# Performance work log

Measured on AMD Instinct MI355X. Metric: run time of the kernel, lower is better.

The kernel has to match this reference:

```python
import jax, jax.numpy as jnp
import numpy as np


def _cft_icft_matrices(n):
    # Continuous FT over t in [0,1) sampled at n points, frequencies = fftfreq(n, d=1/n).
    # CFT  : X(f) = integral x(t) e^{-2pi i f t} dt  ~=  (1/n) * sum_t x(t) e^{-2pi i f t}
    # ICFT : x(t) = integral X(f) e^{+2pi i f t} df  ~=  df   * sum_f X(f) e^{+2pi i f t}
    # The original module evaluates the ICFT on the fftshift-ed frequency grid while the
    # coefficients stay in fft (unshifted) index order; we reproduce that pairing.
    sr = float(n)
    t = jnp.arange(n, dtype=jnp.float32) / n                      # [n]
    f = jnp.fft.fftfreq(n, d=1.0 / sr).astype(jnp.float32)        # [n], fft order
    f_shift = jnp.fft.fftshift(f)                                 # [n], shifted order
    two_pi = jnp.float32(2.0 * np.pi)
    dt = jnp.float32(1.0 / n)
    df = jnp.float32(sr / n)  # frequency spacing = 1.0 for unit duration
    # E_cft: [n_freq, n_time], E_icft: [n_time, n_freq]
    E_cft = jnp.exp(-1j * two_pi * f[:, None] * t[None, :]).astype(jnp.complex64) * dt
    E_icft = jnp.exp(1j * two_pi * t[:, None] * f_shift[None, :]).astype(jnp.complex64) * df
    return E_cft, E_icft


def setup_inputs() -> dict:
    key = jax.random.key(0)
    k1, k2, k3 = jax.random.split(key, 3)
    B, Ci, Co, n, modes = 32, 64, 64, 4096, 64
    scale = 1.0 / (Ci * Co)
    x = jax.random.normal(k1, (B, Ci, n), dtype=jnp.float32)
    # weights1 = scale * rand(Ci, Co, modes, cfloat): uniform[0,1) real and imag parts
    w_real = scale * jax.random.uniform(k2, (Ci, Co, modes), dtype=jnp.float32)
    w_imag = scale * jax.random.uniform(k3, (Ci, Co, modes), dtype=jnp.float32)
    return {"x": x, "w_real": w_real, "w_imag": w_imag}


def reference(x, w_real, w_imag):
    B, Ci, n = x.shape
    Co, modes = w_real.shape[1], w_real.shape[2]
    E_cft, E_icft = _cft_icft_matrices(n)
    w = (w_real + 1j * w_imag).astype(jnp.complex64)              # [Ci, Co, modes]
    xc = x.astype(jnp.complex64)
    # Batched CFT over all (batch, channel) pairs as one complex GEMM.
    x_cft = jnp.einsum('bit,ft->bif', xc, E_cft)                  # [B, Ci, n]
    # Spectral linear transform on the lowest `modes` frequencies.
    low = jnp.einsum('bif,iof->bof', x_cft[:, :, :modes], w)      # [B, Co, modes]
    out_ft = jnp.zeros((B, Co, n), dtype=jnp.complex64).at[:, :, :modes].set(low)
    # Batched ICFT back to the time grid; module returns the real part.
    out = jnp.einsum('bof,tf->bot', out_ft, E_icft)               # [B, Co, n]
    return out.real
```

## Files before the change

### kernel.cpp

```cpp
#include <hip/hip_runtime.h>
#include <math.h>

#define NT 4096
#define MODES 64
#define ROWS 2048
#define TWO_PI 6.283185307179586f

typedef __attribute__((ext_vector_type(8))) short bf16x8;
typedef __attribute__((ext_vector_type(4))) float f32x4;

static __device__ __forceinline__ unsigned short bf16rn(float x) {
  unsigned u = __float_as_uint(x);
  u += 0x7FFFu + ((u >> 16) & 1u);
  return (unsigned short)(u >> 16);
}

__global__ __launch_bounds__(256) void bgen_kernel(unsigned short* __restrict__ Bg,
                                                   unsigned short* __restrict__ Cg) {
  const int bx = (int)blockIdx.x;
  if (bx < 256) {
    const int e0 = (bx * 256 + (int)threadIdx.x) * 8;
    const int n = e0 >> 12;
    const int t0 = e0 & 4095;
    const int k = (n < 64) ? n : (n - 64);
    bf16x8 pack;
#pragma unroll
    for (int j = 0; j < 8; ++j) {
      const int ph = (k * (t0 + j)) & (NT - 1);
      float s, c;
      sincosf(TWO_PI * (float)ph / (float)NT, &s, &c);
      const float v = ((n < 64) ? c : -s) * (1.0f / (float)NT);
      pack[j] = (short)bf16rn(v);
    }
    *(bf16x8*)(Bg + e0) = pack;
  } else {
    const int e0 = ((bx - 256) * 256 + (int)threadIdx.x) * 8;
    const int t = e0 >> 7;
    const int k2b = e0 & 127;
    const float sgn = (t & 1) ? -1.f : 1.f;
    bf16x8 pack;
#pragma unroll
    for (int j = 0; j < 8; ++j) {
      const int k2 = k2b + j;
      const int k = (k2 < 64) ? k2 : (k2 - 64);
      const int ph = (k * t) & (NT - 1);
      float s, c;
      sincosf(TWO_PI * (float)ph / (float)NT, &s, &c);
      const float v = ((k2 < 64) ? c : -s) * sgn;
      pack[j] = (short)bf16rn(v);
    }
    *(bf16x8*)(Cg + e0) = pack;
  }
}

__global__ __launch_bounds__(256) void cft_mfma_kernel(
    const float* __restrict__ x, const unsigned short* __restrict__ Bg,
    float* __restrict__ xfp,
    const float* __restrict__ w_real, const float* __restrict__ w_imag,
    float* __restrict__ wrt, float* __restrict__ wit, int S) {
  __shared__ __align__(16) char smem[24576];
  const int tid = threadIdx.x;
  const int nCft = 64 * S;

  if ((int)blockIdx.x >= nCft) {
    float (*tile)[65] = (float (*)[65])smem;
    const int bx = (int)blockIdx.x - nCft;
    const int sel = bx >> 6;
    const int io0 = (bx & 63) * 64;
    const float* __restrict__ src = sel ? w_imag : w_real;
    float* __restrict__ dst = sel ? wit : wrt;
#pragma unroll
    for (int j = 0; j < 4; ++j) {
      const int idx = tid + j * 256;
      const int r = idx >> 4;
      const int kq = idx & 15;
      float4 v = ((const float4*)src)[(size_t)(io0 + r) * 16 + kq];
      tile[r][4 * kq + 0] = v.x; tile[r][4 * kq + 1] = v.y;
      tile[r][4 * kq + 2] = v.z; tile[r][4 * kq + 3] = v.w;
    }
    __syncthreads();
#pragma unroll
    for (int j = 0; j < 16; ++j) {
      const int idx = tid + j * 256;
      const int k = idx >> 6;
      const int r = idx & 63;
      dst[(size_t)k * 4096 + io0 + r] = tile[r][k];
    }
    return;
  }

  unsigned short* Ah = (unsigned short*)smem;
  unsigned short* Al = (unsigned short*)(smem + 4096);
  unsigned short* Bs = (unsigned short*)(smem + 8192);

  const int rowblk = (int)blockIdx.x / S;
  const int ts = (int)blockIdx.x % S;
  const int row0 = rowblk * 32;
  const int t0 = ts * (NT / S);
  const int subs = (NT / S) / 64;

  const int lane = tid & 63;
  const int w = tid >> 6;

  f32x4 acc[2][2];
#pragma unroll
  for (int mt = 0; mt < 2; ++mt)
#pragma unroll
    for (int nt = 0; nt < 2; ++nt) acc[mt][nt] = (f32x4){0.f, 0.f, 0.f, 0.f};

  const int aru = tid & 7;
  const int arow = tid >> 3;

  for (int sub = 0; sub < subs; ++sub) {
    const int tb = t0 + sub * 64;
    __syncthreads();
    {
      const float* xp = x + (size_t)(row0 + arow) * NT + tb + aru * 8;
      const float4 v0 = *(const float4*)xp;
      const float4 v1 = *(const float4*)(xp + 4);
      float xv[8] = {v0.x, v0.y, v0.z, v0.w, v1.x, v1.y, v1.z, v1.w};
      bf16x8 ph, pl;
#pragma unroll
      for (int j = 0; j < 8; ++j) {
        const unsigned short h = bf16rn(xv[j]);
        ph[j] = (short)h;
        const float hf = __uint_as_float((unsigned)h << 16);
        pl[j] = (short)bf16rn(xv[j] - hf);
      }
      const int col = (aru ^ (arow & 7)) * 8;
      *(bf16x8*)(Ah + arow * 64 + col) = ph;
      *(bf16x8*)(Al + arow * 64 + col) = pl;
    }
#pragma unroll
    for (int it = 0; it < 4; ++it) {
      const int idx = tid + it * 256;
      const int ku = idx & 7;
      const int n = idx >> 3;
      const bf16x8 v = *(const bf16x8*)(Bg + (size_t)n * NT + tb + ku * 8);
      const int col = (ku ^ (n & 7)) * 8;
      *(bf16x8*)(Bs + n * 64 + col) = v;
    }
    __syncthreads();
    const int kg = lane >> 4;
#pragma unroll
    for (int ks = 0; ks < 2; ++ks) {
      bf16x8 bf[2];
#pragma unroll
      for (int nt = 0; nt < 2; ++nt) {
        const int n = w * 32 + nt * 16 + (lane & 15);
        const int col = ((ks * 4 + kg) ^ (n & 7)) * 8;
        bf[nt] = *(const bf16x8*)(Bs + n * 64 + col);
      }
#pragma unroll
      for (int mt = 0; mt < 2; ++mt) {
        const int row = mt * 16 + (lane & 15);
        const int col = ((ks * 4 + kg) ^ (row & 7)) * 8;
        const bf16x8 ah = *(const bf16x8*)(Ah + row * 64 + col);
        const bf16x8 al = *(const bf16x8*)(Al + row * 64 + col);
#pragma unroll
        for (int nt = 0; nt < 2; ++nt) {
          acc[mt][nt] = __builtin_amdgcn_mfma_f32_16x16x32_bf16(ah, bf[nt], acc[mt][nt], 0, 0, 0);
          acc[mt][nt] = __builtin_amdgcn_mfma_f32_16x16x32_bf16(al, bf[nt], acc[mt][nt], 0, 0, 0);
        }
      }
    }
  }
  const int nb = w * 32 + (lane & 15);
#pragma unroll
  for (int nt = 0; nt < 2; ++nt) {
    const int n = nb + nt * 16;
    const int plane = n >> 6;
    const int kk = n & 63;
#pragma unroll
    for (int mt = 0; mt < 2; ++mt) {
      const int rl = mt * 16 + (lane >> 4) * 4;
      float4 st = {acc[mt][nt][0], acc[mt][nt][1], acc[mt][nt][2], acc[mt][nt][3]};
      ((float4*)xfp)[((((size_t)ts * 64 + rowblk) * 2 + plane) * 64 + kk) * 8 + (rl >> 2)] = st;
    }
  }
}

__global__ __launch_bounds__(256) void mix_kernel(
    const float* __restrict__ wrt, const float* __restrict__ wit,
    const float* __restrict__ xfp, float2* __restrict__ yf_t, int S) {
  __shared__ float2 wsc[4096];
  __shared__ float2 xsh[256];
  const int k = blockIdx.x & 63;
  const int bq = blockIdx.x >> 6;
  const int tid = threadIdx.x;
#pragma unroll
  for (int j = 0; j < 4; ++j) {
    const int idx = tid + 256 * j;
    float4 vr = ((const float4*)(wrt + (size_t)k * 4096))[idx];
    float4 vi = ((const float4*)(wit + (size_t)k * 4096))[idx];
    wsc[4 * idx + 0] = make_float2(vr.x, vi.x);
    wsc[4 * idx + 1] = make_float2(vr.y, vi.y);
    wsc[4 * idx + 2] = make_float2(vr.z, vi.z);
    wsc[4 * idx + 3] = make_float2(vr.w, vi.w);
  }
  {
    const int R = bq * 256 + tid;
    const int rowblk = R >> 5;
    const int rl = R & 31;
    float2 acc = make_float2(0.f, 0.f);
    for (int s = 0; s < S; ++s) {
      const size_t b0 = (((size_t)s * 64 + rowblk) * 2) * 2048;
      acc.x += xfp[b0 + (size_t)k * 32 + rl];
      acc.y += xfp[b0 + 2048 + (size_t)k * 32 + rl];
    }
    xsh[tid] = acc;
  }
  __syncthreads();
  const int o = tid & 63;
  const int bl = tid >> 6;
  float accr = 0.f, acci = 0.f;
#pragma unroll 8
  for (int i = 0; i < 64; ++i) {
    const float2 xv = xsh[bl * 64 + i];
    const float2 w = wsc[i * 64 + o];
    accr = fmaf(xv.x, w.x, accr); accr = fmaf(-xv.y, w.y, accr);
    acci = fmaf(xv.x, w.y, acci); acci = fmaf( xv.y, w.x, acci);
  }
  yf_t[(size_t)k * ROWS + bq * 256 + bl * 64 + o] = make_float2(accr, acci);
}

__global__ __launch_bounds__(256) void icft_mfma_kernel(
    const float2* __restrict__ yf_t, const unsigned short* __restrict__ Cg,
    float* __restrict__ out) {
  __shared__ __align__(16) char smem[24576];
  unsigned short* Ay = (unsigned short*)smem;
  unsigned short* Cs = (unsigned short*)(smem + 8192);
  const int tid = threadIdx.x;
  const int rgrp = (int)blockIdx.x >> 4;
  const int tgrp = (int)blockIdx.x & 15;
  const int row0 = rgrp * 32;
  const int tb0 = tgrp * 256;
  const int lane = tid & 63;
  const int w = tid >> 6;

#pragma unroll
  for (int it = 0; it < 8; ++it) {
    const int idx = tid + it * 256;
    const int k = idx >> 5;
    const int rl = idx & 31;
    const float2 y = yf_t[(size_t)k * ROWS + row0 + rl];
    const int ur = (k >> 3) ^ (rl & 7);
    Ay[rl * 128 + ur * 8 + (k & 7)] = bf16rn(y.x);
    Ay[rl * 128 + (8 | ur) * 8 + (k & 7)] = bf16rn(y.y);
  }
  __syncthreads();

  bf16x8 afr[2][4];
#pragma unroll
  for (int mt = 0; mt < 2; ++mt) {
    const int row = mt * 16 + (lane & 15);
#pragma unroll
    for (int ks = 0; ks < 4; ++ks) {
      const int unit = ks * 4 + (lane >> 4);
      const int cu = unit ^ (row & 7);
      afr[mt][ks] = *(const bf16x8*)(Ay + row * 128 + cu * 8);
    }
  }

  for (int sub = 0; sub < 4; ++sub) {
    const int tb = tb0 + sub * 64;
    __syncthreads();
#pragma unroll
    for (int it = 0; it < 4; ++it) {
      const int idx = tid + it * 256;
      const int ku = idx & 15;
      const int tl = idx >> 4;
      const bf16x8 v = *(const bf16x8*)(Cg + (size_t)(tb + tl) * 128 + ku * 8);
      Cs[tl * 128 + (ku ^ (tl & 7)) * 8] = 0;
      *(bf16x8*)(Cs + tl * 128 + (ku ^ (tl & 7)) * 8) = v;
    }
    __syncthreads();
    const int tl = w * 16 + (lane & 15);
    f32x4 acc[2];
    acc[0] = (f32x4){0.f, 0.f, 0.f, 0.f};
    acc[1] = (f32x4){0.f, 0.f, 0.f, 0.f};
#pragma unroll
    for (int ks = 0; ks < 4; ++ks) {
      const int unit = ks * 4 + (lane >> 4);
      const int cu = unit ^ (tl & 7);
      const bf16x8 bf = *(const bf16x8*)(Cs + tl * 128 + cu * 8);
      acc[0] = __builtin_amdgcn_mfma_f32_16x16x32_bf16(afr[0][ks], bf, acc[0], 0, 0, 0);
      acc[1] = __builtin_amdgcn_mfma_f32_16x16x32_bf16(afr[1][ks], bf, acc[1], 0, 0, 0);
    }
    const int t = tb + tl;
#pragma unroll
    for (int mt = 0; mt < 2; ++mt) {
      const int rbase = row0 + mt * 16 + (lane >> 4) * 4;
#pragma unroll
      for (int reg = 0; reg < 4; ++reg) {
        out[(size_t)(rbase + reg) * NT + t] = acc[mt][reg];
      }
    }
  }
}

extern "C" void kernel_launch(void* const* d_in, const int* in_sizes, int n_in,
                              void* d_out, int out_size, void* d_ws, size_t ws_size,
                              hipStream_t stream) {
  const float* x      = (const float*)d_in[0];
  const float* w_real = (const float*)d_in[1];
  const float* w_imag = (const float*)d_in[2];
  float* out = (float*)d_out;

  const size_t MB = (size_t)ROWS * MODES * sizeof(float2);
  int S = 16;
  while (S > 4 && (size_t)(S + 6) * MB > ws_size) S >>= 1;

  char* wsp = (char*)d_ws;
  float*  xfp  = (float*)wsp;
  float2* yf_t = (float2*)(wsp + (size_t)S * MB);
  float*  wrt  = (float*)(wsp + (size_t)(S + 2) * MB);
  float*  wit  = (float*)(wsp + (size_t)(S + 3) * MB);
  unsigned short* Bg = (unsigned short*)(wsp + (size_t)(S + 4) * MB);
  unsigned short* Cg = (unsigned short*)(wsp + (size_t)(S + 5) * MB);

  bgen_kernel<<<512, 256, 0, stream>>>(Bg, Cg);
  cft_mfma_kernel<<<64 * S + 128, 256, 0, stream>>>(x, Bg, xfp, w_real, w_imag,
                                                    wrt, wit, S);
  mix_kernel<<<512, 256, 0, stream>>>(wrt, wit, xfp, yf_t, S);
  icft_mfma_kernel<<<1024, 256, 0, stream>>>(yf_t, Cg, out);
}
```

Measured before the change: 42.76 us.

## Load B/C operand fragments directly from global instead of staging in LDS

Both the CFT and ICFT MFMA kernels now read the basis-matrix operand fragments straight from global memory into registers, with no LDS staging. This drops the LDS stores and reads and shrinks shared-memory use. The CFT time-split factor S also drops from 16 to 8, so there are fewer, longer blocks and fewer partial sums for the mix kernel to reduce. The risk is that each wave's global loads are less coalesced and are repeated across waves, which leans on L1/L2 to serve the reused basis data.

```diff
diff --git a/kernel.cpp b/kernel.cpp
--- a/kernel.cpp
+++ b/kernel.cpp
@@ -58,7 +58,7 @@
     float* __restrict__ xfp,
     const float* __restrict__ w_real, const float* __restrict__ w_imag,
     float* __restrict__ wrt, float* __restrict__ wit, int S) {
-  __shared__ __align__(16) char smem[24576];
+  __shared__ __align__(16) char smem[16896];
   const int tid = threadIdx.x;
   const int nCft = 64 * S;
 
@@ -91,7 +91,6 @@
 
   unsigned short* Ah = (unsigned short*)smem;
   unsigned short* Al = (unsigned short*)(smem + 4096);
-  unsigned short* Bs = (unsigned short*)(smem + 8192);
 
   const int rowblk = (int)blockIdx.x / S;
   const int ts = (int)blockIdx.x % S;
@@ -110,6 +109,7 @@
 
   const int aru = tid & 7;
   const int arow = tid >> 3;
+  const int kg = lane >> 4;
 
   for (int sub = 0; sub < subs; ++sub) {
     const int tb = t0 + sub * 64;
@@ -131,25 +131,14 @@
       *(bf16x8*)(Ah + arow * 64 + col) = ph;
       *(bf16x8*)(Al + arow * 64 + col) = pl;
     }
-#pragma unroll
-    for (int it = 0; it < 4; ++it) {
-      const int idx = tid + it * 256;
-      const int ku = idx & 7;
-      const int n = idx >> 3;
-      const bf16x8 v = *(const bf16x8*)(Bg + (size_t)n * NT + tb + ku * 8);
-      const int col = (ku ^ (n & 7)) * 8;
-      *(bf16x8*)(Bs + n * 64 + col) = v;
-    }
     __syncthreads();
-    const int kg = lane >> 4;
 #pragma unroll
     for (int ks = 0; ks < 2; ++ks) {
       bf16x8 bf[2];
 #pragma unroll
       for (int nt = 0; nt < 2; ++nt) {
         const int n = w * 32 + nt * 16 + (lane & 15);
-        const int col = ((ks * 4 + kg) ^ (n & 7)) * 8;
-        bf[nt] = *(const bf16x8*)(Bs + n * 64 + col);
+        bf[nt] = *(const bf16x8*)(Bg + (size_t)n * NT + tb + (ks * 4 + kg) * 8);
       }
 #pragma unroll
       for (int mt = 0; mt < 2; ++mt) {
@@ -227,9 +216,7 @@
 __global__ __launch_bounds__(256) void icft_mfma_kernel(
     const float2* __restrict__ yf_t, const unsigned short* __restrict__ Cg,
     float* __restrict__ out) {
-  __shared__ __align__(16) char smem[24576];
-  unsigned short* Ay = (unsigned short*)smem;
-  unsigned short* Cs = (unsigned short*)(smem + 8192);
+  __shared__ __align__(16) unsigned short Ay[32 * 128];
   const int tid = threadIdx.x;
   const int rgrp = (int)blockIdx.x >> 4;
   const int tgrp = (int)blockIdx.x & 15;
@@ -262,32 +249,19 @@
     }
   }
 
+  const int tl = w * 16 + (lane & 15);
   for (int sub = 0; sub < 4; ++sub) {
-    const int tb = tb0 + sub * 64;
-    __syncthreads();
-#pragma unroll
-    for (int it = 0; it < 4; ++it) {
-      const int idx = tid + it * 256;
-      const int ku = idx & 15;
-      const int tl = idx >> 4;
-      const bf16x8 v = *(const bf16x8*)(Cg + (size_t)(tb + tl) * 128 + ku * 8);
-      Cs[tl * 128 + (ku ^ (tl & 7)) * 8] = 0;
-      *(bf16x8*)(Cs + tl * 128 + (ku ^ (tl & 7)) * 8) = v;
-    }
-    __syncthreads();
-    const int tl = w * 16 + (lane & 15);
+    const int t = tb0 + sub * 64 + tl;
     f32x4 acc[2];
     acc[0] = (f32x4){0.f, 0.f, 0.f, 0.f};
     acc[1] = (f32x4){0.f, 0.f, 0.f, 0.f};
 #pragma unroll
     for (int ks = 0; ks < 4; ++ks) {
       const int unit = ks * 4 + (lane >> 4);
-      const int cu = unit ^ (tl & 7);
-      const bf16x8 bf = *(const bf16x8*)(Cs + tl * 128 + cu * 8);
+      const bf16x8 bf = *(const bf16x8*)(Cg + (size_t)t * 128 + unit * 8);
       acc[0] = __builtin_amdgcn_mfma_f32_16x16x32_bf16(afr[0][ks], bf, acc[0], 0, 0, 0);
       acc[1] = __builtin_amdgcn_mfma_f32_16x16x32_bf16(afr[1][ks], bf, acc[1], 0, 0, 0);
     }
-    const int t = tb + tl;
 #pragma unroll
     for (int mt = 0; mt < 2; ++mt) {
       const int rbase = row0 + mt * 16 + (lane >> 4) * 4;
@@ -308,7 +282,7 @@
   float* out = (float*)d_out;
 
   const size_t MB = (size_t)ROWS * MODES * sizeof(float2);
-  int S = 16;
+  int S = 8;
   while (S > 4 && (size_t)(S + 6) * MB > ws_size) S >>= 1;
 
   char* wsp = (char*)d_ws;
```

After: 47.37 us. 1.11x slower.
